# Optimization experiments

Hardware: AMD Instinct MI355X
Metric: run time of the kernel (lower is better)

## Reference

```python
import jax, jax.numpy as jnp
import numpy as np

N_SRC = 100000
N_DST = 100000
E = 500000
D = 128      # in_units
F = 64       # efeat_dim
NB = 2       # num_basis
C = 5        # num_classes


def setup_inputs() -> dict:
    key = jax.random.key(0)
    ks = jax.random.split(key, 14)
    s = 1.0 / np.sqrt(D)
    return {
        "h_src": jax.random.normal(ks[0], (N_SRC, D), jnp.float32),
        "h_dst": jax.random.normal(ks[1], (N_DST, D), jnp.float32),
        "efeats": jax.random.normal(ks[2], (E, F), jnp.float32),
        "u_idx": jax.random.randint(ks[3], (E,), 0, N_SRC),
        "v_idx": jax.random.randint(ks[4], (E,), 0, N_DST),
        "W1": jax.random.normal(ks[5], (D, F), jnp.float32) * (1.0 / np.sqrt(F)),
        "b1": jnp.zeros((D,), jnp.float32),
        "W2": jax.random.normal(ks[6], (D, D), jnp.float32) * s,
        "b2": jnp.zeros((D,), jnp.float32),
        "W3": jax.random.normal(ks[7], (D, D), jnp.float32) * s,
        "b3": jnp.zeros((D,), jnp.float32),
        "W_comb": jax.random.normal(ks[8], (D, 2 * D), jnp.float32) * (1.0 / np.sqrt(2 * D)),
        "P": jax.random.normal(ks[9], (NB, D, D), jnp.float32) * s,
        "W_cb": jax.random.normal(ks[10], (C, NB), jnp.float32) * (1.0 / np.sqrt(NB)),
    }


def reference(h_src, h_dst, efeats, u_idx, v_idx,
              W1, b1, W2, b2, W3, b3, W_comb, P, W_cb):
    # 3-layer edge-feature MLP (dropout is identity at eval / rate=0)
    e = jax.nn.relu(efeats @ W1.T + b1)   # [E, D]
    e = jax.nn.relu(e @ W2.T + b2)        # [E, D]
    e = e @ W3.T + b3                     # [E, D]
    # gather node feats by edge endpoints, concat with transformed efeats, combine
    u = jnp.concatenate([h_src[u_idx], e], axis=1) @ W_comb.T  # [E, D]
    v = jnp.concatenate([h_dst[v_idx], e], axis=1) @ W_comb.T  # [E, D]
    # bilinear basis decode: out[e, b] = u[e] @ P[b] @ v[e]
    out = jnp.einsum('ei,bij,ej->eb', u, P, v)  # [E, NB]
    return out @ W_cb.T                          # [E, C]
```

## Files before the change

kernel.cpp:

```cpp
#include <hip/hip_runtime.h>
#include <hip/hip_bf16.h>

#define NNODE 100000
#define EDG   500000
#define DD    128
#define FF    64
#define NCLS  5

#define OFF_W1   0
#define OFF_W2   8192
#define OFF_W3   24576
#define OFF_WCR  40960
#define OFF_WCL  57344
#define OFF_P0   73728
#define OFF_P1   90112
#define OFF_HU   106496
#define OFF_HV   (106496 + NNODE * DD)
#define PREP_TOT 106496

typedef __attribute__((ext_vector_type(8))) short short8;
typedef __attribute__((ext_vector_type(4))) float f32x4;

union U4 { uint4 v; ushort s[8]; };

__device__ __forceinline__ float bf2f(ushort u) {
  return __uint_as_float(((unsigned int)u) << 16);
}
__device__ __forceinline__ ushort f2bf(float f) {
  unsigned int u = __float_as_uint(f);
  u += 0x7FFF + ((u >> 16) & 1);
  return (ushort)(u >> 16);
}
__device__ __forceinline__ ushort2 pk2(float a, float b) {
  __hip_bfloat162 t = __float22bfloat162_rn(make_float2(a, b));
  return *(ushort2*)&t;
}
__device__ __forceinline__ ushort4 pk4(float a, float b, float c, float d) {
  ushort2 lo = pk2(a, b), hi = pk2(c, d);
  ushort4 o; o.x = lo.x; o.y = lo.y; o.z = hi.x; o.w = hi.y; return o;
}

__device__ __forceinline__ int sw(int row, int col) {
  return row * 128 + ((((col >> 3) ^ (row & 7)) << 3) | (col & 7));
}


template <int NT>
__device__ __forceinline__ void gemm_T1(const ushort* act,
                                        const ushort* __restrict__ W, int K,
                                        int ksteps, f32x4 acc[NT],
                                        int m0, int l15, int q) {
  for (int ks = 0; ks < ksteps; ++ks) {
    const int ko = ks * 32 + q * 8;
    short8 a0 = *(const short8*)(W + (m0 + l15) * K + ko);
#pragma unroll
    for (int nt = 0; nt < NT; ++nt) {
      short8 b = *(const short8*)&act[sw(nt * 16 + l15, ko)];
      acc[nt] = __builtin_amdgcn_mfma_f32_16x16x32_bf16(a0, b, acc[nt], 0, 0, 0);
    }
  }
}

template <int NT>
__device__ __forceinline__ void zaccN(f32x4 a[NT]) {
#pragma unroll
  for (int j = 0; j < NT; ++j) a[j] = (f32x4){0.f, 0.f, 0.f, 0.f};
}

template <int NT>
__device__ __forceinline__ void store_T1(ushort* dst, f32x4 acc[NT],
                                         const float* __restrict__ bias, int relu,
                                         int m0, int l15, int q) {
  const int feat = m0 + q * 4;
  float4 bv = bias ? *(const float4*)(bias + feat) : make_float4(0.f, 0.f, 0.f, 0.f);
#pragma unroll
  for (int nt = 0; nt < NT; ++nt) {
    const int edge = nt * 16 + l15;
    float v0 = acc[nt][0] + bv.x, v1 = acc[nt][1] + bv.y;
    float v2 = acc[nt][2] + bv.z, v3 = acc[nt][3] + bv.w;
    if (relu) {
      v0 = fmaxf(v0, 0.f); v1 = fmaxf(v1, 0.f);
      v2 = fmaxf(v2, 0.f); v3 = fmaxf(v3, 0.f);
    }
    *(ushort4*)&dst[sw(edge, feat)] = pk4(v0, v1, v2, v3);
  }
}

__global__ void __launch_bounds__(256) prep_kernel(
    const float* __restrict__ W1, const float* __restrict__ W2,
    const float* __restrict__ W3, const float* __restrict__ W_comb,
    const float* __restrict__ P, ushort* __restrict__ ws) {
  int idx = blockIdx.x * 256 + threadIdx.x;
  if (idx >= PREP_TOT) return;
  float val;
  if (idx < 8192) {
    val = W1[idx];
  } else {
    int r = idx - 8192, m = r >> 14, rr = r & 16383;
    switch (m) {
      case 0:  val = W2[rr]; break;
      case 1:  val = W3[rr]; break;
      case 2:  { int n = rr >> 7, k = rr & 127; val = W_comb[n * 256 + 128 + k]; } break;
      case 3:  { int n = rr >> 7, k = rr & 127; val = W_comb[n * 256 + k]; } break;
      case 4:  val = P[rr]; break;
      default: val = P[16384 + rr]; break;
    }
  }
  ws[idx] = f2bf(val);
}

__global__ void __launch_bounds__(512, 4) node_kernel(
    const float* __restrict__ h_src, const float* __restrict__ h_dst,
    ushort* __restrict__ ws) {
  __shared__ ushort BUF[2][128][128];
  ushort* A = &BUF[0][0][0];
  ushort* B = &BUF[1][0][0];
  const int NTIL = (NNODE + 127) / 128;
  const int tid = threadIdx.x;
  const int lane = tid & 63, l15 = lane & 15, q = lane >> 4;
  const int m0 = (tid >> 6) * 16;
  const int bb = blockIdx.x;
  const float* h = (bb < NTIL) ? h_src : h_dst;
  ushort* op = ws + ((bb < NTIL) ? OFF_HU : OFF_HV);
  const int r0 = ((bb < NTIL) ? bb : bb - NTIL) * 128;
  const int srow = tid >> 2, part = tid & 3;
  int row = r0 + srow; if (row >= NNODE) row = NNODE - 1;
  {
    const float4* src = (const float4*)(h + (long)row * DD) + part * 8;
#pragma unroll
    for (int c = 0; c < 4; ++c) {
      float4 v0 = src[c * 2], v1 = src[c * 2 + 1];
      U4 o;
      *(ushort4*)&o.s[0] = pk4(v0.x, v0.y, v0.z, v0.w);
      *(ushort4*)&o.s[4] = pk4(v1.x, v1.y, v1.z, v1.w);
      *(uint4*)&A[sw(srow, part * 32 + c * 8)] = o.v;
    }
  }
  __syncthreads();
  f32x4 acc[8];
  zaccN<8>(acc);
  gemm_T1<8>(A, ws + OFF_WCL, 128, 4, acc, m0, l15, q);
  store_T1<8>(B, acc, nullptr, 0, m0, l15, q);
  __syncthreads();
  if (r0 + srow < NNODE) {
    uint4* d = (uint4*)(op + (long)(r0 + srow) * DD + part * 32);
#pragma unroll
    for (int i = 0; i < 4; ++i)
      d[i] = *(const uint4*)&B[sw(srow, part * 32 + i * 8)];
  }
}

__global__ void __launch_bounds__(512, 4) edge_kernel(
    const float* __restrict__ efeats, const int* __restrict__ u_idx,
    const int* __restrict__ v_idx, const float* __restrict__ b1,
    const float* __restrict__ b2, const float* __restrict__ b3,
    const float* __restrict__ W_cb, const ushort* __restrict__ ws,
    float* __restrict__ out) {
  __shared__ ushort BUF[2][128][128];
  __shared__ float OB[128][2];
  ushort* A = &BUF[0][0][0];
  ushort* B = &BUF[1][0][0];

  const int tid = threadIdx.x;
  const int lane = tid & 63;
  const int l15 = lane & 15, q = lane >> 4;
  const int m0 = (tid >> 6) * 16;
  const long e0 = (long)blockIdx.x * 128;

  const int srow = tid >> 2, part = tid & 3;
  long grow = e0 + srow; if (grow >= EDG) grow = EDG - 1;
  const int vi = v_idx[grow], ui = u_idx[grow];

  {
    const float4* src = (const float4*)(efeats + grow * FF) + part * 4;
#pragma unroll
    for (int c = 0; c < 2; ++c) {
      float4 v0 = src[c * 2], v1 = src[c * 2 + 1];
      U4 o;
      *(ushort4*)&o.s[0] = pk4(v0.x, v0.y, v0.z, v0.w);
      *(ushort4*)&o.s[4] = pk4(v1.x, v1.y, v1.z, v1.w);
      *(uint4*)&A[sw(srow, part * 16 + c * 8)] = o.v;
    }
  }
  __syncthreads();

  f32x4 acc[8];
  zaccN<8>(acc); gemm_T1<8>(A, ws + OFF_W1, 64, 2, acc, m0, l15, q);
  store_T1<8>(B, acc, b1, 1, m0, l15, q);
  __syncthreads();
  zaccN<8>(acc); gemm_T1<8>(B, ws + OFF_W2, 128, 4, acc, m0, l15, q);
  store_T1<8>(A, acc, b2, 1, m0, l15, q);
  __syncthreads();
  zaccN<8>(acc); gemm_T1<8>(A, ws + OFF_W3, 128, 4, acc, m0, l15, q);
  store_T1<8>(B, acc, b3, 0, m0, l15, q);
  __syncthreads();

  uint4 hvp[4];
  {
    const uint4* hp = (const uint4*)(ws + OFF_HV + (long)vi * DD) + part * 4;
#pragma unroll
    for (int c = 0; c < 4; ++c) hvp[c] = hp[c];
  }
  zaccN<8>(acc); gemm_T1<8>(B, ws + OFF_WCR, 128, 4, acc, m0, l15, q);
  store_T1<8>(A, acc, nullptr, 0, m0, l15, q);
  __syncthreads();

  {
#pragma unroll
    for (int c = 0; c < 4; ++c) {
      U4 a; a.v = hvp[c];
      U4 e; e.v = *(const uint4*)&A[sw(srow, part * 32 + c * 8)];
      U4 o;
#pragma unroll
      for (int j = 0; j < 8; j += 2) {
        ushort2 p = pk2(bf2f(a.s[j]) + bf2f(e.s[j]),
                        bf2f(a.s[j + 1]) + bf2f(e.s[j + 1]));
        o.s[j] = p.x; o.s[j + 1] = p.y;
      }
      *(uint4*)&B[sw(srow, part * 32 + c * 8)] = o.v;
    }
    if (tid < 256) OB[tid >> 1][tid & 1] = 0.f;
  }
  __syncthreads();

  uint4 hup[4];
  {
    const uint4* hp = (const uint4*)(ws + OFF_HU + (long)ui * DD) + part * 4;
#pragma unroll
    for (int c = 0; c < 4; ++c) hup[c] = hp[c];
  }

  f32x4 tacc[2][8];
  zaccN<8>(tacc[0]); zaccN<8>(tacc[1]);
  for (int ks = 0; ks < 4; ++ks) {
    const int ko = ks * 32 + q * 8;
    short8 a0 = *(const short8*)(ws + OFF_P0 + (m0 + l15) * 128 + ko);
    short8 a1 = *(const short8*)(ws + OFF_P1 + (m0 + l15) * 128 + ko);
#pragma unroll
    for (int nt = 0; nt < 8; ++nt) {
      short8 b = *(const short8*)&B[sw(nt * 16 + l15, ko)];
      tacc[0][nt] = __builtin_amdgcn_mfma_f32_16x16x32_bf16(a0, b, tacc[0][nt], 0, 0, 0);
      tacc[1][nt] = __builtin_amdgcn_mfma_f32_16x16x32_bf16(a1, b, tacc[1][nt], 0, 0, 0);
    }
  }
  __syncthreads();

  {
#pragma unroll
    for (int c = 0; c < 4; ++c) {
      U4 a; a.v = hup[c];
      U4 e; e.v = *(const uint4*)&A[sw(srow, part * 32 + c * 8)];
      U4 o;
#pragma unroll
      for (int j = 0; j < 8; j += 2) {
        ushort2 p = pk2(bf2f(a.s[j]) + bf2f(e.s[j]),
                        bf2f(a.s[j + 1]) + bf2f(e.s[j + 1]));
        o.s[j] = p.x; o.s[j + 1] = p.y;
      }
      *(uint4*)&B[sw(srow, part * 32 + c * 8)] = o.v;
    }
  }
  __syncthreads();

#pragma unroll
  for (int nt = 0; nt < 8; ++nt) {
    const int edge = nt * 16 + l15;
    float pb0 = 0.f, pb1 = 0.f;
    ushort4 u4 = *(const ushort4*)&B[sw(edge, m0 + q * 4)];
    float uf;
    uf = bf2f(u4.x); pb0 += tacc[0][nt][0] * uf; pb1 += tacc[1][nt][0] * uf;
    uf = bf2f(u4.y); pb0 += tacc[0][nt][1] * uf; pb1 += tacc[1][nt][1] * uf;
    uf = bf2f(u4.z); pb0 += tacc[0][nt][2] * uf; pb1 += tacc[1][nt][2] * uf;
    uf = bf2f(u4.w); pb0 += tacc[0][nt][3] * uf; pb1 += tacc[1][nt][3] * uf;
    pb0 += __shfl_xor(pb0, 16, 64); pb0 += __shfl_xor(pb0, 32, 64);
    pb1 += __shfl_xor(pb1, 16, 64); pb1 += __shfl_xor(pb1, 32, 64);
    if (q == 0) {
      atomicAdd(&OB[edge][0], pb0);
      atomicAdd(&OB[edge][1], pb1);
    }
  }
  __syncthreads();

  for (int t = tid; t < 128 * NCLS; t += 512) {
    int r = t / NCLS, c = t % NCLS;
    long erow = e0 + r;
    if (erow < EDG) {
      out[erow * NCLS + c] = OB[r][0] * W_cb[c * 2] + OB[r][1] * W_cb[c * 2 + 1];
    }
  }
}

extern "C" void kernel_launch(void* const* d_in, const int* in_sizes, int n_in,
                              void* d_out, int out_size, void* d_ws,
                              size_t ws_size, hipStream_t stream) {
  const float* h_src  = (const float*)d_in[0];
  const float* h_dst  = (const float*)d_in[1];
  const float* efeats = (const float*)d_in[2];
  const int*   u_idx  = (const int*)d_in[3];
  const int*   v_idx  = (const int*)d_in[4];
  const float* W1     = (const float*)d_in[5];
  const float* b1     = (const float*)d_in[6];
  const float* W2     = (const float*)d_in[7];
  const float* b2     = (const float*)d_in[8];
  const float* W3     = (const float*)d_in[9];
  const float* b3     = (const float*)d_in[10];
  const float* W_comb = (const float*)d_in[11];
  const float* P      = (const float*)d_in[12];
  const float* W_cb   = (const float*)d_in[13];
  ushort* ws = (ushort*)d_ws;
  float* out = (float*)d_out;

  prep_kernel<<<(PREP_TOT + 255) / 256, 256, 0, stream>>>(W1, W2, W3, W_comb, P, ws);
  node_kernel<<<2 * ((NNODE + 127) / 128), 512, 0, stream>>>(h_src, h_dst, ws);
  edge_kernel<<<(EDG + 127) / 128, 512, 0, stream>>>(efeats, u_idx, v_idx,
                                                     b1, b2, b3, W_cb, ws, out);
}
```

Before: 450.3 us.

## Keep combined edge projection in registers, gather node rows in MFMA layout

The shared W_comb-right projection stays in accumulator registers, and the gathered h_dst/h_src projections are added directly in the MFMA output layout. This removes two shared-memory round trips and two barriers. The u vector is kept in fp32 registers instead of being rounded to bf16. The P transform is split into two halves to bound register pressure. Index loads move earlier to overlap with the W3 GEMM, but node-row gathers now use 8-byte loads per lane instead of 16-byte contiguous chunks, which may coalesce worse.

```diff
diff --git a/kernel.cpp b/kernel.cpp
--- a/kernel.cpp
+++ b/kernel.cpp
@@ -22,6 +22,7 @@
 typedef __attribute__((ext_vector_type(4))) float f32x4;
 
 union U4 { uint4 v; ushort s[8]; };
+union U2 { uint2 v; ushort s[4]; };
 
 __device__ __forceinline__ float bf2f(ushort u) {
   return __uint_as_float(((unsigned int)u) << 16);
@@ -169,7 +170,6 @@
 
   const int srow = tid >> 2, part = tid & 3;
   long grow = e0 + srow; if (grow >= EDG) grow = EDG - 1;
-  const int vi = v_idx[grow], ui = u_idx[grow];
 
   {
     const float4* src = (const float4*)(efeats + grow * FF) + part * 4;
@@ -191,92 +191,72 @@
   zaccN<8>(acc); gemm_T1<8>(B, ws + OFF_W2, 128, 4, acc, m0, l15, q);
   store_T1<8>(A, acc, b2, 1, m0, l15, q);
   __syncthreads();
+
+  int vidx[8], uidx[8];
+#pragma unroll
+  for (int nt = 0; nt < 8; ++nt) {
+    long g = e0 + nt * 16 + l15; if (g >= EDG) g = EDG - 1;
+    vidx[nt] = v_idx[g]; uidx[nt] = u_idx[g];
+  }
+
   zaccN<8>(acc); gemm_T1<8>(A, ws + OFF_W3, 128, 4, acc, m0, l15, q);
   store_T1<8>(B, acc, b3, 0, m0, l15, q);
   __syncthreads();
 
-  uint4 hvp[4];
-  {
-    const uint4* hp = (const uint4*)(ws + OFF_HV + (long)vi * DD) + part * 4;
-#pragma unroll
-    for (int c = 0; c < 4; ++c) hvp[c] = hp[c];
-  }
+  U2 hvf[8], huf[8];
+#pragma unroll
+  for (int nt = 0; nt < 8; ++nt) {
+    hvf[nt].v = *(const uint2*)(ws + OFF_HV + (long)vidx[nt] * DD + m0 + q * 4);
+    huf[nt].v = *(const uint2*)(ws + OFF_HU + (long)uidx[nt] * DD + m0 + q * 4);
+  }
+
   zaccN<8>(acc); gemm_T1<8>(B, ws + OFF_WCR, 128, 4, acc, m0, l15, q);
-  store_T1<8>(A, acc, nullptr, 0, m0, l15, q);
-  __syncthreads();
-
-  {
-#pragma unroll
-    for (int c = 0; c < 4; ++c) {
-      U4 a; a.v = hvp[c];
-      U4 e; e.v = *(const uint4*)&A[sw(srow, part * 32 + c * 8)];
-      U4 o;
-#pragma unroll
-      for (int j = 0; j < 8; j += 2) {
-        ushort2 p = pk2(bf2f(a.s[j]) + bf2f(e.s[j]),
-                        bf2f(a.s[j + 1]) + bf2f(e.s[j + 1]));
-        o.s[j] = p.x; o.s[j + 1] = p.y;
-      }
-      *(uint4*)&B[sw(srow, part * 32 + c * 8)] = o.v;
-    }
-    if (tid < 256) OB[tid >> 1][tid & 1] = 0.f;
-  }
-  __syncthreads();
-
-  uint4 hup[4];
-  {
-    const uint4* hp = (const uint4*)(ws + OFF_HU + (long)ui * DD) + part * 4;
-#pragma unroll
-    for (int c = 0; c < 4; ++c) hup[c] = hp[c];
-  }
-
-  f32x4 tacc[2][8];
-  zaccN<8>(tacc[0]); zaccN<8>(tacc[1]);
-  for (int ks = 0; ks < 4; ++ks) {
-    const int ko = ks * 32 + q * 8;
-    short8 a0 = *(const short8*)(ws + OFF_P0 + (m0 + l15) * 128 + ko);
-    short8 a1 = *(const short8*)(ws + OFF_P1 + (m0 + l15) * 128 + ko);
-#pragma unroll
-    for (int nt = 0; nt < 8; ++nt) {
-      short8 b = *(const short8*)&B[sw(nt * 16 + l15, ko)];
-      tacc[0][nt] = __builtin_amdgcn_mfma_f32_16x16x32_bf16(a0, b, tacc[0][nt], 0, 0, 0);
-      tacc[1][nt] = __builtin_amdgcn_mfma_f32_16x16x32_bf16(a1, b, tacc[1][nt], 0, 0, 0);
-    }
-  }
-  __syncthreads();
-
-  {
-#pragma unroll
-    for (int c = 0; c < 4; ++c) {
-      U4 a; a.v = hup[c];
-      U4 e; e.v = *(const uint4*)&A[sw(srow, part * 32 + c * 8)];
-      U4 o;
-#pragma unroll
-      for (int j = 0; j < 8; j += 2) {
-        ushort2 p = pk2(bf2f(a.s[j]) + bf2f(e.s[j]),
-                        bf2f(a.s[j + 1]) + bf2f(e.s[j + 1]));
-        o.s[j] = p.x; o.s[j + 1] = p.y;
-      }
-      *(uint4*)&B[sw(srow, part * 32 + c * 8)] = o.v;
-    }
-  }
-  __syncthreads();
 
 #pragma unroll
   for (int nt = 0; nt < 8; ++nt) {
     const int edge = nt * 16 + l15;
-    float pb0 = 0.f, pb1 = 0.f;
-    ushort4 u4 = *(const ushort4*)&B[sw(edge, m0 + q * 4)];
-    float uf;
-    uf = bf2f(u4.x); pb0 += tacc[0][nt][0] * uf; pb1 += tacc[1][nt][0] * uf;
-    uf = bf2f(u4.y); pb0 += tacc[0][nt][1] * uf; pb1 += tacc[1][nt][1] * uf;
-    uf = bf2f(u4.z); pb0 += tacc[0][nt][2] * uf; pb1 += tacc[1][nt][2] * uf;
-    uf = bf2f(u4.w); pb0 += tacc[0][nt][3] * uf; pb1 += tacc[1][nt][3] * uf;
-    pb0 += __shfl_xor(pb0, 16, 64); pb0 += __shfl_xor(pb0, 32, 64);
-    pb1 += __shfl_xor(pb1, 16, 64); pb1 += __shfl_xor(pb1, 32, 64);
-    if (q == 0) {
-      atomicAdd(&OB[edge][0], pb0);
-      atomicAdd(&OB[edge][1], pb1);
+    float v0 = acc[nt][0] + bf2f(hvf[nt].s[0]);
+    float v1 = acc[nt][1] + bf2f(hvf[nt].s[1]);
+    float v2 = acc[nt][2] + bf2f(hvf[nt].s[2]);
+    float v3 = acc[nt][3] + bf2f(hvf[nt].s[3]);
+    *(ushort4*)&A[sw(edge, m0 + q * 4)] = pk4(v0, v1, v2, v3);
+    acc[nt][0] += bf2f(huf[nt].s[0]);
+    acc[nt][1] += bf2f(huf[nt].s[1]);
+    acc[nt][2] += bf2f(huf[nt].s[2]);
+    acc[nt][3] += bf2f(huf[nt].s[3]);
+  }
+  if (tid < 256) OB[tid >> 1][tid & 1] = 0.f;
+  __syncthreads();
+
+#pragma unroll
+  for (int h = 0; h < 2; ++h) {
+    f32x4 t0[4], t1[4];
+    zaccN<4>(t0); zaccN<4>(t1);
+    for (int ks = 0; ks < 4; ++ks) {
+      const int ko = ks * 32 + q * 8;
+      short8 a0 = *(const short8*)(ws + OFF_P0 + (m0 + l15) * 128 + ko);
+      short8 a1 = *(const short8*)(ws + OFF_P1 + (m0 + l15) * 128 + ko);
+#pragma unroll
+      for (int j = 0; j < 4; ++j) {
+        short8 b = *(const short8*)&A[sw((h * 4 + j) * 16 + l15, ko)];
+        t0[j] = __builtin_amdgcn_mfma_f32_16x16x32_bf16(a0, b, t0[j], 0, 0, 0);
+        t1[j] = __builtin_amdgcn_mfma_f32_16x16x32_bf16(a1, b, t1[j], 0, 0, 0);
+      }
+    }
+#pragma unroll
+    for (int j = 0; j < 4; ++j) {
+      const int nt = h * 4 + j;
+      const int edge = nt * 16 + l15;
+      float pb0 = t0[j][0] * acc[nt][0] + t0[j][1] * acc[nt][1]
+                + t0[j][2] * acc[nt][2] + t0[j][3] * acc[nt][3];
+      float pb1 = t1[j][0] * acc[nt][0] + t1[j][1] * acc[nt][1]
+                + t1[j][2] * acc[nt][2] + t1[j][3] * acc[nt][3];
+      pb0 += __shfl_xor(pb0, 16, 64); pb0 += __shfl_xor(pb0, 32, 64);
+      pb1 += __shfl_xor(pb1, 16, 64); pb1 += __shfl_xor(pb1, 32, 64);
+      if (q == 0) {
+        atomicAdd(&OB[edge][0], pb0);
+        atomicAdd(&OB[edge][1], pb1);
+      }
     }
   }
   __syncthreads();
```

New measurement: 474.3 us. 1.05x slower.
